# Kernel tuning notes

Measured on AMD Instinct MI355X. Metric: run time of the kernel, lower is better.

The kernel has to match this reference:

```python
import jax, jax.numpy as jnp
import numpy as np

N = 50000       # nodes
E = 800000      # edges (avg degree 16)
DIN = 128
DOUT = 128
ALPHA = 0.2     # leaky relu negative slope


def setup_inputs() -> dict:
    key = jax.random.key(0)
    k1, k2, k3, k4, k5 = jax.random.split(key, 5)
    h = jax.random.normal(k1, (N, DIN), dtype=jnp.float32)
    # xavier-normal-ish scaling for params
    W = jax.random.normal(k2, (DIN, DOUT), dtype=jnp.float32) * np.float32(np.sqrt(2.0 / (DIN + DOUT)))
    a = jax.random.normal(k3, (2 * DOUT,), dtype=jnp.float32) * np.float32(np.sqrt(2.0 / (2 * DOUT + 1)))
    src = jax.random.randint(k4, (E,), 0, N, dtype=jnp.int32)
    dst = jax.random.randint(k5, (E,), 0, N, dtype=jnp.int32)
    return {"h": h, "W": W, "a": a, "src": src, "dst": dst}


def reference(h, W, a, src, dst):
    # eval mode: dropout is a no-op (training=False)
    Wh = h @ W                                  # [N, DOUT]
    a_src, a_dst = a[:DOUT], a[DOUT:]
    s = Wh @ a_src                              # [N] per-node src score
    d = Wh @ a_dst                              # [N] per-node dst score
    e = jax.nn.leaky_relu(s[src] + d[dst], negative_slope=ALPHA)  # [E]
    # segment softmax over incoming edges of each dst node
    emax = jax.ops.segment_max(e, dst, num_segments=N)            # [N]
    emax = jnp.where(jnp.isfinite(emax), emax, jnp.float32(0.0))  # isolated nodes
    ex = jnp.exp(e - emax[dst])                                   # [E]
    denom = jax.ops.segment_sum(ex, dst, num_segments=N)          # [N]
    alpha = ex / denom[dst]                                       # [E]
    # weighted scatter-sum of src features into dst nodes
    h_out = jax.ops.segment_sum(alpha[:, None] * Wh[src], dst, num_segments=N)  # [N, DOUT]
    # residual: in_feats == out_feats -> Identity
    return h_out + h
```

## Files before the change

### kernel.cpp

```cpp
#include <hip/hip_runtime.h>
#include <math.h>

#define NN 50000
#define NE 800000
#define DD 128
#define LRELU 0.2f
#define CAP 64
#define SLICE 6256

typedef unsigned int uint;

__device__ __forceinline__ uint pack_bf2(float x, float y) {
  uint a = __float_as_uint(x), b = __float_as_uint(y);
  a = (a + 0x7fffu + ((a >> 16) & 1u)) >> 16;
  b = (b + 0x7fffu + ((b >> 16) & 1u)) >> 16;
  return a | (b << 16);
}

__global__ __launch_bounds__(256) void k_gemm(const float* __restrict__ h,
                                              const float* __restrict__ W,
                                              const float* __restrict__ a,
                                              uint* __restrict__ Whb,
                                              float* __restrict__ sv,
                                              float* __restrict__ dv,
                                              int* __restrict__ cnt) {
  __shared__ float hs[32][64];
  __shared__ float Ws[32][128];
  const int tid = threadIdx.x;
  const int brow = blockIdx.x * 64;

  if (tid < 64) {
    int idx = blockIdx.x * 64 + tid;
    if (idx < NN) cnt[idx] = 0;
  }

  const int tx = tid & 15, ty = tid >> 4;
  const int c0 = tx * 4, c1 = 64 + tx * 4;
  float acc[4][8];
#pragma unroll
  for (int r = 0; r < 4; ++r)
#pragma unroll
    for (int j = 0; j < 8; ++j) acc[r][j] = 0.f;

  const int lr = tid >> 2;
  const int lc = (tid & 3) * 8;
  int grow = brow + lr; if (grow >= NN) grow = 0;

  for (int k0 = 0; k0 < DD; k0 += 32) {
    {
      const float4* hp = reinterpret_cast<const float4*>(h + (size_t)grow * DD + k0 + lc);
      float4 v0 = hp[0], v1 = hp[1];
      hs[lc + 0][lr] = v0.x; hs[lc + 1][lr] = v0.y;
      hs[lc + 2][lr] = v0.z; hs[lc + 3][lr] = v0.w;
      hs[lc + 4][lr] = v1.x; hs[lc + 5][lr] = v1.y;
      hs[lc + 6][lr] = v1.z; hs[lc + 7][lr] = v1.w;
    }
#pragma unroll
    for (int i = 0; i < 4; ++i) {
      int f = i * 256 + tid;
      int kk = f >> 5, cc = (f & 31) * 4;
      *reinterpret_cast<float4*>(&Ws[kk][cc]) =
          *reinterpret_cast<const float4*>(W + (size_t)(k0 + kk) * DD + cc);
    }
    __syncthreads();
#pragma unroll
    for (int k = 0; k < 32; ++k) {
      float4 av = *reinterpret_cast<const float4*>(&hs[k][ty * 4]);
      float4 b0 = *reinterpret_cast<const float4*>(&Ws[k][c0]);
      float4 b1 = *reinterpret_cast<const float4*>(&Ws[k][c1]);
      acc[0][0] = fmaf(av.x, b0.x, acc[0][0]); acc[0][1] = fmaf(av.x, b0.y, acc[0][1]);
      acc[0][2] = fmaf(av.x, b0.z, acc[0][2]); acc[0][3] = fmaf(av.x, b0.w, acc[0][3]);
      acc[0][4] = fmaf(av.x, b1.x, acc[0][4]); acc[0][5] = fmaf(av.x, b1.y, acc[0][5]);
      acc[0][6] = fmaf(av.x, b1.z, acc[0][6]); acc[0][7] = fmaf(av.x, b1.w, acc[0][7]);
      acc[1][0] = fmaf(av.y, b0.x, acc[1][0]); acc[1][1] = fmaf(av.y, b0.y, acc[1][1]);
      acc[1][2] = fmaf(av.y, b0.z, acc[1][2]); acc[1][3] = fmaf(av.y, b0.w, acc[1][3]);
      acc[1][4] = fmaf(av.y, b1.x, acc[1][4]); acc[1][5] = fmaf(av.y, b1.y, acc[1][5]);
      acc[1][6] = fmaf(av.y, b1.z, acc[1][6]); acc[1][7] = fmaf(av.y, b1.w, acc[1][7]);
      acc[2][0] = fmaf(av.z, b0.x, acc[2][0]); acc[2][1] = fmaf(av.z, b0.y, acc[2][1]);
      acc[2][2] = fmaf(av.z, b0.z, acc[2][2]); acc[2][3] = fmaf(av.z, b0.w, acc[2][3]);
      acc[2][4] = fmaf(av.z, b1.x, acc[2][4]); acc[2][5] = fmaf(av.z, b1.y, acc[2][5]);
      acc[2][6] = fmaf(av.z, b1.z, acc[2][6]); acc[2][7] = fmaf(av.z, b1.w, acc[2][7]);
      acc[3][0] = fmaf(av.w, b0.x, acc[3][0]); acc[3][1] = fmaf(av.w, b0.y, acc[3][1]);
      acc[3][2] = fmaf(av.w, b0.z, acc[3][2]); acc[3][3] = fmaf(av.w, b0.w, acc[3][3]);
      acc[3][4] = fmaf(av.w, b1.x, acc[3][4]); acc[3][5] = fmaf(av.w, b1.y, acc[3][5]);
      acc[3][6] = fmaf(av.w, b1.z, acc[3][6]); acc[3][7] = fmaf(av.w, b1.w, acc[3][7]);
    }
    __syncthreads();
  }

  float4 as0 = *reinterpret_cast<const float4*>(a + c0);
  float4 as1 = *reinterpret_cast<const float4*>(a + c1);
  float4 ad0 = *reinterpret_cast<const float4*>(a + DD + c0);
  float4 ad1 = *reinterpret_cast<const float4*>(a + DD + c1);
#pragma unroll
  for (int r = 0; r < 4; ++r) {
    int row = brow + ty * 4 + r;
    bool ok = row < NN;
    if (ok) {
      uint2 p0 = make_uint2(pack_bf2(acc[r][0], acc[r][1]), pack_bf2(acc[r][2], acc[r][3]));
      uint2 p1 = make_uint2(pack_bf2(acc[r][4], acc[r][5]), pack_bf2(acc[r][6], acc[r][7]));
      *reinterpret_cast<uint2*>(Whb + (size_t)row * 64 + c0 / 2) = p0;
      *reinterpret_cast<uint2*>(Whb + (size_t)row * 64 + c1 / 2) = p1;
    }
    float ps = acc[r][0] * as0.x + acc[r][1] * as0.y + acc[r][2] * as0.z + acc[r][3] * as0.w
             + acc[r][4] * as1.x + acc[r][5] * as1.y + acc[r][6] * as1.z + acc[r][7] * as1.w;
    float pd = acc[r][0] * ad0.x + acc[r][1] * ad0.y + acc[r][2] * ad0.z + acc[r][3] * ad0.w
             + acc[r][4] * ad1.x + acc[r][5] * ad1.y + acc[r][6] * ad1.z + acc[r][7] * ad1.w;
#pragma unroll
    for (int off = 8; off > 0; off >>= 1) {
      ps += __shfl_xor(ps, off);
      pd += __shfl_xor(pd, off);
    }
    if (tx == 0 && ok) { sv[row] = ps; dv[row] = pd; }
  }
}

__global__ __launch_bounds__(256) void k_fill(const int* __restrict__ src,
                                              const int* __restrict__ dst,
                                              const float* __restrict__ sv,
                                              const float* __restrict__ dv,
                                              int* __restrict__ cnt,
                                              uint2* __restrict__ entries) {
  const int xcd = blockIdx.x & 7;
  const int e0 = (blockIdx.x >> 3) * 3125;
  const int e1 = e0 + 3125;
  for (int i = e0 + threadIdx.x; i < e1; i += 256) {
    int d = dst[i];
    if (d / SLICE != xcd) continue;
    int s = src[i];
    float ev = sv[s] + dv[d];
    ev = ev > 0.f ? ev : LRELU * ev;
    float x = __expf(ev);
    int p = atomicAdd(&cnt[d], 1);
    if (p < CAP) entries[(size_t)d * CAP + p] = make_uint2((uint)s, __float_as_uint(x));
  }
}

__global__ __launch_bounds__(256) void k_node(const float* __restrict__ h,
                                              const uint* __restrict__ Whb,
                                              const int* __restrict__ cnt,
                                              const uint2* __restrict__ entries,
                                              float* __restrict__ out) {
  const int sl = blockIdx.x & 7;
  int wid = sl * SLICE + (blockIdx.x >> 3) * 4 + (threadIdx.x >> 6);
  const int lim = min(NN, (sl + 1) * SLICE);
  if (wid >= lim) return;
  wid = __builtin_amdgcn_readfirstlane(wid);
  const int lane = threadIdx.x & 63;

  float2 hrow = reinterpret_cast<const float2*>(h + (size_t)wid * DD)[lane];
  int deg = cnt[wid];
  deg = deg < CAP ? deg : CAP;
  float2* o2 = reinterpret_cast<float2*>(out + (size_t)wid * DD);
  if (deg == 0) { o2[lane] = hrow; return; }

  const uint2* bucket = entries + (size_t)wid * CAP;
  float2 accA = make_float2(0.f, 0.f);
  float2 accB = make_float2(0.f, 0.f);
  float den = 0.f;
  int k = 0;
  for (; k + 2 <= deg; k += 2) {
    uint2 q0 = bucket[k], q1 = bucket[k + 1];
    float x0 = __uint_as_float(q0.y), x1 = __uint_as_float(q1.y);
    den += x0 + x1;
    uint u0 = Whb[(size_t)q0.x * 64 + lane];
    uint u1 = Whb[(size_t)q1.x * 64 + lane];
    accA.x = fmaf(x0, __uint_as_float(u0 << 16), accA.x);
    accA.y = fmaf(x0, __uint_as_float(u0 & 0xffff0000u), accA.y);
    accB.x = fmaf(x1, __uint_as_float(u1 << 16), accB.x);
    accB.y = fmaf(x1, __uint_as_float(u1 & 0xffff0000u), accB.y);
  }
  if (k < deg) {
    uint2 q0 = bucket[k];
    float x0 = __uint_as_float(q0.y);
    den += x0;
    uint u0 = Whb[(size_t)q0.x * 64 + lane];
    accA.x = fmaf(x0, __uint_as_float(u0 << 16), accA.x);
    accA.y = fmaf(x0, __uint_as_float(u0 & 0xffff0000u), accA.y);
  }
  float inv = 1.0f / den;
  o2[lane] = make_float2(hrow.x + (accA.x + accB.x) * inv,
                         hrow.y + (accA.y + accB.y) * inv);
}

extern "C" void kernel_launch(void* const* d_in, const int* in_sizes, int n_in,
                              void* d_out, int out_size, void* d_ws, size_t ws_size,
                              hipStream_t stream) {
  const float* h = (const float*)d_in[0];
  const float* W = (const float*)d_in[1];
  const float* a = (const float*)d_in[2];
  const int* src = (const int*)d_in[3];
  const int* dst = (const int*)d_in[4];
  float* out = (float*)d_out;

  char* ws = (char*)d_ws;
  uint*  Whb     = (uint*) (ws);
  float* sv      = (float*)(ws + 12800000);
  float* dv      = (float*)(ws + 13000000);
  int*   cnt     = (int*)  (ws + 13200000);
  uint2* entries = (uint2*)(ws + 13400000);

  hipLaunchKernelGGL(k_gemm, dim3((NN + 63) / 64), dim3(256), 0, stream,
                     h, W, a, Whb, sv, dv, cnt);
  hipLaunchKernelGGL(k_fill, dim3(2048), dim3(256), 0, stream,
                     src, dst, sv, dv, cnt, entries);
  hipLaunchKernelGGL(k_node, dim3(8 * ((SLICE + 3) / 4)), dim3(256), 0, stream,
                     h, Whb, cnt, entries, out);
}
```

Baseline: 185.5 us.

## Split GEMM into bf16 MFMA kernel, precompute W·a scores, compress edge entries

The FP32 shared-memory GEMM is replaced by several kernels. A single-block prep folds W·a into per-feature score vectors and writes a transposed bf16 copy of W. A light kernel computes the src/dst scores directly from h and casts h to bf16. A new kernel computes Wh with bf16 MFMA 16x16x32 instructions, reading W from swizzled LDS. Edge entries shrink to 4 bytes, holding a 16-bit source index and a bf16 exp weight, and k_fill and k_node are unrolled by 4 for more memory-level parallelism. This lowers GEMM and entry traffic at the cost of precision, an extra pass over h, and a serial single-block prep kernel. The 16-bit index relies on N being at most 65536.

```diff
diff --git a/kernel.cpp b/kernel.cpp
--- a/kernel.cpp
+++ b/kernel.cpp
@@ -9,6 +9,9 @@
 #define SLICE 6256
 
 typedef unsigned int uint;
+typedef unsigned short ushort;
+using short8 = __attribute__((ext_vector_type(8))) short;
+using f32x4  = __attribute__((ext_vector_type(4))) float;
 
 __device__ __forceinline__ uint pack_bf2(float x, float y) {
   uint a = __float_as_uint(x), b = __float_as_uint(y);
@@ -16,102 +19,123 @@
   b = (b + 0x7fffu + ((b >> 16) & 1u)) >> 16;
   return a | (b << 16);
 }
-
-__global__ __launch_bounds__(256) void k_gemm(const float* __restrict__ h,
-                                              const float* __restrict__ W,
+__device__ __forceinline__ ushort pack_bf1(float x) {
+  uint a = __float_as_uint(x);
+  return (ushort)((a + 0x7fffu + ((a >> 16) & 1u)) >> 16);
+}
+
+__global__ __launch_bounds__(256) void k_prep(const float* __restrict__ W,
                                               const float* __restrict__ a,
-                                              uint* __restrict__ Whb,
+                                              float* __restrict__ wsv,
+                                              float* __restrict__ wdv,
+                                              ushort* __restrict__ Wtg) {
+  const int tid = threadIdx.x;
+  if (tid < DD) {
+    float accs = 0.f, accd = 0.f;
+    for (int c = 0; c < DD; ++c) {
+      float w = W[tid * DD + c];
+      accs = fmaf(w, a[c], accs);
+      accd = fmaf(w, a[DD + c], accd);
+    }
+    wsv[tid] = accs;
+    wdv[tid] = accd;
+  }
+  for (int i = 0; i < 64; ++i) {
+    int idx = tid * 64 + i;
+    int c = idx >> 7, k = idx & 127;
+    Wtg[idx] = pack_bf1(W[k * DD + c]);
+  }
+}
+
+__global__ __launch_bounds__(256) void k_svdv(const float* __restrict__ h,
+                                              const float* __restrict__ wsv,
+                                              const float* __restrict__ wdv,
                                               float* __restrict__ sv,
                                               float* __restrict__ dv,
+                                              ushort* __restrict__ h_b,
                                               int* __restrict__ cnt) {
-  __shared__ float hs[32][64];
-  __shared__ float Ws[32][128];
   const int tid = threadIdx.x;
-  const int brow = blockIdx.x * 64;
-
-  if (tid < 64) {
-    int idx = blockIdx.x * 64 + tid;
-    if (idx < NN) cnt[idx] = 0;
-  }
-
-  const int tx = tid & 15, ty = tid >> 4;
-  const int c0 = tx * 4, c1 = 64 + tx * 4;
-  float acc[4][8];
-#pragma unroll
-  for (int r = 0; r < 4; ++r)
-#pragma unroll
-    for (int j = 0; j < 8; ++j) acc[r][j] = 0.f;
-
-  const int lr = tid >> 2;
-  const int lc = (tid & 3) * 8;
-  int grow = brow + lr; if (grow >= NN) grow = 0;
-
-  for (int k0 = 0; k0 < DD; k0 += 32) {
-    {
-      const float4* hp = reinterpret_cast<const float4*>(h + (size_t)grow * DD + k0 + lc);
-      float4 v0 = hp[0], v1 = hp[1];
-      hs[lc + 0][lr] = v0.x; hs[lc + 1][lr] = v0.y;
-      hs[lc + 2][lr] = v0.z; hs[lc + 3][lr] = v0.w;
-      hs[lc + 4][lr] = v1.x; hs[lc + 5][lr] = v1.y;
-      hs[lc + 6][lr] = v1.z; hs[lc + 7][lr] = v1.w;
-    }
-#pragma unroll
-    for (int i = 0; i < 4; ++i) {
-      int f = i * 256 + tid;
-      int kk = f >> 5, cc = (f & 31) * 4;
-      *reinterpret_cast<float4*>(&Ws[kk][cc]) =
-          *reinterpret_cast<const float4*>(W + (size_t)(k0 + kk) * DD + cc);
-    }
-    __syncthreads();
-#pragma unroll
-    for (int k = 0; k < 32; ++k) {
-      float4 av = *reinterpret_cast<const float4*>(&hs[k][ty * 4]);
-      float4 b0 = *reinterpret_cast<const float4*>(&Ws[k][c0]);
-      float4 b1 = *reinterpret_cast<const float4*>(&Ws[k][c1]);
-      acc[0][0] = fmaf(av.x, b0.x, acc[0][0]); acc[0][1] = fmaf(av.x, b0.y, acc[0][1]);
-      acc[0][2] = fmaf(av.x, b0.z, acc[0][2]); acc[0][3] = fmaf(av.x, b0.w, acc[0][3]);
-      acc[0][4] = fmaf(av.x, b1.x, acc[0][4]); acc[0][5] = fmaf(av.x, b1.y, acc[0][5]);
-      acc[0][6] = fmaf(av.x, b1.z, acc[0][6]); acc[0][7] = fmaf(av.x, b1.w, acc[0][7]);
-      acc[1][0] = fmaf(av.y, b0.x, acc[1][0]); acc[1][1] = fmaf(av.y, b0.y, acc[1][1]);
-      acc[1][2] = fmaf(av.y, b0.z, acc[1][2]); acc[1][3] = fmaf(av.y, b0.w, acc[1][3]);
-      acc[1][4] = fmaf(av.y, b1.x, acc[1][4]); acc[1][5] = fmaf(av.y, b1.y, acc[1][5]);
-      acc[1][6] = fmaf(av.y, b1.z, acc[1][6]); acc[1][7] = fmaf(av.y, b1.w, acc[1][7]);
-      acc[2][0] = fmaf(av.z, b0.x, acc[2][0]); acc[2][1] = fmaf(av.z, b0.y, acc[2][1]);
-      acc[2][2] = fmaf(av.z, b0.z, acc[2][2]); acc[2][3] = fmaf(av.z, b0.w, acc[2][3]);
-      acc[2][4] = fmaf(av.z, b1.x, acc[2][4]); acc[2][5] = fmaf(av.z, b1.y, acc[2][5]);
-      acc[2][6] = fmaf(av.z, b1.z, acc[2][6]); acc[2][7] = fmaf(av.z, b1.w, acc[2][7]);
-      acc[3][0] = fmaf(av.w, b0.x, acc[3][0]); acc[3][1] = fmaf(av.w, b0.y, acc[3][1]);
-      acc[3][2] = fmaf(av.w, b0.z, acc[3][2]); acc[3][3] = fmaf(av.w, b0.w, acc[3][3]);
-      acc[3][4] = fmaf(av.w, b1.x, acc[3][4]); acc[3][5] = fmaf(av.w, b1.y, acc[3][5]);
-      acc[3][6] = fmaf(av.w, b1.z, acc[3][6]); acc[3][7] = fmaf(av.w, b1.w, acc[3][7]);
-    }
-    __syncthreads();
-  }
-
-  float4 as0 = *reinterpret_cast<const float4*>(a + c0);
-  float4 as1 = *reinterpret_cast<const float4*>(a + c1);
-  float4 ad0 = *reinterpret_cast<const float4*>(a + DD + c0);
-  float4 ad1 = *reinterpret_cast<const float4*>(a + DD + c1);
-#pragma unroll
-  for (int r = 0; r < 4; ++r) {
-    int row = brow + ty * 4 + r;
-    bool ok = row < NN;
-    if (ok) {
-      uint2 p0 = make_uint2(pack_bf2(acc[r][0], acc[r][1]), pack_bf2(acc[r][2], acc[r][3]));
-      uint2 p1 = make_uint2(pack_bf2(acc[r][4], acc[r][5]), pack_bf2(acc[r][6], acc[r][7]));
-      *reinterpret_cast<uint2*>(Whb + (size_t)row * 64 + c0 / 2) = p0;
-      *reinterpret_cast<uint2*>(Whb + (size_t)row * 64 + c1 / 2) = p1;
-    }
-    float ps = acc[r][0] * as0.x + acc[r][1] * as0.y + acc[r][2] * as0.z + acc[r][3] * as0.w
-             + acc[r][4] * as1.x + acc[r][5] * as1.y + acc[r][6] * as1.z + acc[r][7] * as1.w;
-    float pd = acc[r][0] * ad0.x + acc[r][1] * ad0.y + acc[r][2] * ad0.z + acc[r][3] * ad0.w
-             + acc[r][4] * ad1.x + acc[r][5] * ad1.y + acc[r][6] * ad1.z + acc[r][7] * ad1.w;
-#pragma unroll
-    for (int off = 8; off > 0; off >>= 1) {
-      ps += __shfl_xor(ps, off);
-      pd += __shfl_xor(pd, off);
-    }
-    if (tx == 0 && ok) { sv[row] = ps; dv[row] = pd; }
+  if (tid < 16) cnt[blockIdx.x * 16 + tid] = 0;
+  const int wave = tid >> 6, l = tid & 63;
+  const int r = blockIdx.x * 16 + wave * 4 + (l >> 4);
+  const int c8 = (l & 15) * 8;
+  float4 h0 = *reinterpret_cast<const float4*>(h + (size_t)r * DD + c8);
+  float4 h1 = *reinterpret_cast<const float4*>(h + (size_t)r * DD + c8 + 4);
+  float4 w0 = *reinterpret_cast<const float4*>(wsv + c8);
+  float4 w1 = *reinterpret_cast<const float4*>(wsv + c8 + 4);
+  float4 d0 = *reinterpret_cast<const float4*>(wdv + c8);
+  float4 d1 = *reinterpret_cast<const float4*>(wdv + c8 + 4);
+  float ps = h0.x*w0.x + h0.y*w0.y + h0.z*w0.z + h0.w*w0.w
+           + h1.x*w1.x + h1.y*w1.y + h1.z*w1.z + h1.w*w1.w;
+  float pd = h0.x*d0.x + h0.y*d0.y + h0.z*d0.z + h0.w*d0.w
+           + h1.x*d1.x + h1.y*d1.y + h1.z*d1.z + h1.w*d1.w;
+#pragma unroll
+  for (int off = 1; off < 16; off <<= 1) {
+    ps += __shfl_xor(ps, off);
+    pd += __shfl_xor(pd, off);
+  }
+  if ((l & 15) == 0) { sv[r] = ps; dv[r] = pd; }
+  uint4 u;
+  u.x = pack_bf2(h0.x, h0.y); u.y = pack_bf2(h0.z, h0.w);
+  u.z = pack_bf2(h1.x, h1.y); u.w = pack_bf2(h1.z, h1.w);
+  *reinterpret_cast<uint4*>(h_b + (size_t)r * DD + c8) = u;
+}
+
+__global__ __launch_bounds__(256) void k_mfma(const ushort* __restrict__ h_b,
+                                              const ushort* __restrict__ Wtg,
+                                              uint* __restrict__ Whb) {
+  __shared__ ushort WtS[16384];
+  __shared__ float stage[4][16][18];
+  const int tid = threadIdx.x;
+
+#pragma unroll
+  for (int it = 0; it < 16; ++it) {
+    int chunk = it * 256 + tid;
+    int c = chunk >> 4, kc = chunk & 15;
+    short8 v = *reinterpret_cast<const short8*>(Wtg + chunk * 8);
+    *reinterpret_cast<short8*>(
+        reinterpret_cast<char*>(WtS) + c * 256 + ((kc ^ (c & 7)) << 4)) = v;
+  }
+  __syncthreads();
+
+  const int wave = tid >> 6, lane = tid & 63;
+  const int rbase = blockIdx.x * 64 + wave * 16;
+  const int arow = rbase + (lane & 15);
+  const int asrc = arow < NN ? arow : 0;
+  const bool rok = arow < NN;
+
+  short8 afr[4];
+#pragma unroll
+  for (int kg = 0; kg < 4; ++kg)
+    afr[kg] = *reinterpret_cast<const short8*>(
+        h_b + (size_t)asrc * DD + kg * 32 + (lane >> 4) * 8);
+
+  const int xb = lane & 7;
+  for (int cb = 0; cb < 8; ++cb) {
+    const int col = cb * 16 + (lane & 15);
+    f32x4 acc = {0.f, 0.f, 0.f, 0.f};
+#pragma unroll
+    for (int kg = 0; kg < 4; ++kg) {
+      int kchunk = kg * 4 + (lane >> 4);
+      short8 bfr = *reinterpret_cast<const short8*>(
+          reinterpret_cast<const char*>(WtS) + col * 256 + ((kchunk ^ xb) << 4));
+      acc = __builtin_amdgcn_mfma_f32_16x16x32_bf16(afr[kg], bfr, acc, 0, 0, 0);
+    }
+    float (*st)[18] = stage[wave];
+#pragma unroll
+    for (int j = 0; j < 4; ++j) st[(lane >> 4) * 4 + j][lane & 15] = acc[j];
+    __asm__ volatile("s_waitcnt lgkmcnt(0)" ::: "memory");
+    __builtin_amdgcn_sched_barrier(0);
+    if (rok) {
+#pragma unroll
+      for (int j2 = 0; j2 < 2; ++j2) {
+        int p = (lane >> 4) + 4 * j2;
+        float2 v = *reinterpret_cast<const float2*>(&st[lane & 15][2 * p]);
+        Whb[(size_t)arow * 64 + cb * 8 + p] = pack_bf2(v.x, v.y);
+      }
+    }
+    __asm__ volatile("s_waitcnt lgkmcnt(0)" ::: "memory");
+    __builtin_amdgcn_sched_barrier(0);
   }
 }
 
@@ -120,26 +144,52 @@
                                               const float* __restrict__ sv,
                                               const float* __restrict__ dv,
                                               int* __restrict__ cnt,
-                                              uint2* __restrict__ entries) {
+                                              uint* __restrict__ entries) {
   const int xcd = blockIdx.x & 7;
+  const int base = xcd * SLICE;
   const int e0 = (blockIdx.x >> 3) * 3125;
   const int e1 = e0 + 3125;
-  for (int i = e0 + threadIdx.x; i < e1; i += 256) {
-    int d = dst[i];
-    if (d / SLICE != xcd) continue;
-    int s = src[i];
-    float ev = sv[s] + dv[d];
-    ev = ev > 0.f ? ev : LRELU * ev;
-    float x = __expf(ev);
-    int p = atomicAdd(&cnt[d], 1);
-    if (p < CAP) entries[(size_t)d * CAP + p] = make_uint2((uint)s, __float_as_uint(x));
+  const int t = threadIdx.x;
+
+  for (int j0 = 0; j0 < 13; j0 += 4) {
+    int idx[4], d[4];
+    bool keep[4];
+#pragma unroll
+    for (int jj = 0; jj < 4; ++jj) {
+      idx[jj] = e0 + (j0 + jj) * 256 + t;
+      bool valid = idx[jj] < e1;
+      d[jj] = valid ? dst[idx[jj]] : -1;
+      keep[jj] = valid && ((uint)(d[jj] - base) < (uint)SLICE);
+    }
+    int s[4];
+    float x[4];
+#pragma unroll
+    for (int jj = 0; jj < 4; ++jj)
+      s[jj] = keep[jj] ? src[idx[jj]] : 0;
+#pragma unroll
+    for (int jj = 0; jj < 4; ++jj) {
+      if (keep[jj]) {
+        float ev = sv[s[jj]] + dv[d[jj]];
+        ev = ev > 0.f ? ev : LRELU * ev;
+        x[jj] = __expf(ev);
+      }
+    }
+    int p[4];
+#pragma unroll
+    for (int jj = 0; jj < 4; ++jj)
+      if (keep[jj]) p[jj] = atomicAdd(&cnt[d[jj]], 1);
+#pragma unroll
+    for (int jj = 0; jj < 4; ++jj)
+      if (keep[jj] && p[jj] < CAP)
+        entries[(size_t)d[jj] * CAP + p[jj]] =
+            ((uint)pack_bf1(x[jj]) << 16) | (uint)s[jj];
   }
 }
 
 __global__ __launch_bounds__(256) void k_node(const float* __restrict__ h,
                                               const uint* __restrict__ Whb,
                                               const int* __restrict__ cnt,
-                                              const uint2* __restrict__ entries,
+                                              const uint* __restrict__ entries,
                                               float* __restrict__ out) {
   const int sl = blockIdx.x & 7;
   int wid = sl * SLICE + (blockIdx.x >> 3) * 4 + (threadIdx.x >> 6);
@@ -154,33 +204,43 @@
   float2* o2 = reinterpret_cast<float2*>(out + (size_t)wid * DD);
   if (deg == 0) { o2[lane] = hrow; return; }
 
-  const uint2* bucket = entries + (size_t)wid * CAP;
-  float2 accA = make_float2(0.f, 0.f);
-  float2 accB = make_float2(0.f, 0.f);
+  const uint* bucket = entries + (size_t)wid * CAP;
+  const uint4* b4 = reinterpret_cast<const uint4*>(bucket);
+  float2 ac0 = {0.f,0.f}, ac1 = {0.f,0.f}, ac2 = {0.f,0.f}, ac3 = {0.f,0.f};
   float den = 0.f;
-  int k = 0;
-  for (; k + 2 <= deg; k += 2) {
-    uint2 q0 = bucket[k], q1 = bucket[k + 1];
-    float x0 = __uint_as_float(q0.y), x1 = __uint_as_float(q1.y);
-    den += x0 + x1;
-    uint u0 = Whb[(size_t)q0.x * 64 + lane];
-    uint u1 = Whb[(size_t)q1.x * 64 + lane];
-    accA.x = fmaf(x0, __uint_as_float(u0 << 16), accA.x);
-    accA.y = fmaf(x0, __uint_as_float(u0 & 0xffff0000u), accA.y);
-    accB.x = fmaf(x1, __uint_as_float(u1 << 16), accB.x);
-    accB.y = fmaf(x1, __uint_as_float(u1 & 0xffff0000u), accB.y);
-  }
-  if (k < deg) {
-    uint2 q0 = bucket[k];
-    float x0 = __uint_as_float(q0.y);
+  const int nq = deg >> 2;
+  for (int q = 0; q < nq; ++q) {
+    uint4 e4 = b4[q];
+    float x0 = __uint_as_float(e4.x & 0xffff0000u);
+    float x1 = __uint_as_float(e4.y & 0xffff0000u);
+    float x2 = __uint_as_float(e4.z & 0xffff0000u);
+    float x3 = __uint_as_float(e4.w & 0xffff0000u);
+    uint u0 = Whb[(size_t)(e4.x & 0xffffu) * 64 + lane];
+    uint u1 = Whb[(size_t)(e4.y & 0xffffu) * 64 + lane];
+    uint u2 = Whb[(size_t)(e4.z & 0xffffu) * 64 + lane];
+    uint u3 = Whb[(size_t)(e4.w & 0xffffu) * 64 + lane];
+    den += (x0 + x1) + (x2 + x3);
+    ac0.x = fmaf(x0, __uint_as_float(u0 << 16), ac0.x);
+    ac0.y = fmaf(x0, __uint_as_float(u0 & 0xffff0000u), ac0.y);
+    ac1.x = fmaf(x1, __uint_as_float(u1 << 16), ac1.x);
+    ac1.y = fmaf(x1, __uint_as_float(u1 & 0xffff0000u), ac1.y);
+    ac2.x = fmaf(x2, __uint_as_float(u2 << 16), ac2.x);
+    ac2.y = fmaf(x2, __uint_as_float(u2 & 0xffff0000u), ac2.y);
+    ac3.x = fmaf(x3, __uint_as_float(u3 << 16), ac3.x);
+    ac3.y = fmaf(x3, __uint_as_float(u3 & 0xffff0000u), ac3.y);
+  }
+  for (int k = nq * 4; k < deg; ++k) {
+    uint e = bucket[k];
+    float x0 = __uint_as_float(e & 0xffff0000u);
+    uint u0 = Whb[(size_t)(e & 0xffffu) * 64 + lane];
     den += x0;
-    uint u0 = Whb[(size_t)q0.x * 64 + lane];
-    accA.x = fmaf(x0, __uint_as_float(u0 << 16), accA.x);
-    accA.y = fmaf(x0, __uint_as_float(u0 & 0xffff0000u), accA.y);
+    ac0.x = fmaf(x0, __uint_as_float(u0 << 16), ac0.x);
+    ac0.y = fmaf(x0, __uint_as_float(u0 & 0xffff0000u), ac0.y);
   }
   float inv = 1.0f / den;
-  o2[lane] = make_float2(hrow.x + (accA.x + accB.x) * inv,
-                         hrow.y + (accA.y + accB.y) * inv);
+  float ax = (ac0.x + ac1.x) + (ac2.x + ac3.x);
+  float ay = (ac0.y + ac1.y) + (ac2.y + ac3.y);
+  o2[lane] = make_float2(hrow.x + ax * inv, hrow.y + ay * inv);
 }
 
 extern "C" void kernel_launch(void* const* d_in, const int* in_sizes, int n_in,
@@ -194,16 +254,22 @@
   float* out = (float*)d_out;
 
   char* ws = (char*)d_ws;
-  uint*  Whb     = (uint*) (ws);
-  float* sv      = (float*)(ws + 12800000);
-  float* dv      = (float*)(ws + 13000000);
-  int*   cnt     = (int*)  (ws + 13200000);
-  uint2* entries = (uint2*)(ws + 13400000);
-
-  hipLaunchKernelGGL(k_gemm, dim3((NN + 63) / 64), dim3(256), 0, stream,
-                     h, W, a, Whb, sv, dv, cnt);
+  uint*   Whb     = (uint*)  (ws);
+  ushort* h_b     = (ushort*)(ws + 12800000);
+  uint*   entries = (uint*)  (ws + 25600000);
+  ushort* Wtg     = (ushort*)(ws + 38400000);
+  float*  sv      = (float*) (ws + 38432768);
+  float*  dv      = (float*) (ws + 38632768);
+  float*  wsv     = (float*) (ws + 38832768);
+  float*  wdv     = (float*) (ws + 38833280);
+  int*    cnt     = (int*)   (ws + 38833792);
+
+  hipLaunchKernelGGL(k_prep, dim3(1), dim3(256), 0, stream, W, a, wsv, wdv, Wtg);
+  hipLaunchKernelGGL(k_svdv, dim3(3125), dim3(256), 0, stream,
+                     h, wsv, wdv, sv, dv, h_b, cnt);
   hipLaunchKernelGGL(k_fill, dim3(2048), dim3(256), 0, stream,
                      src, dst, sv, dv, cnt, entries);
-  hipLaunchKernelGGL(k_node, dim3(8 * ((SLICE + 3) / 4)), dim3(256), 0, stream,
+  hipLaunchKernelGGL(k_mfma, dim3(782), dim3(256), 0, stream, h_b, Wtg, Whb);
+  hipLaunchKernelGGL(k_node, dim3(8 * (SLICE / 4)), dim3(256), 0, stream,
                      h, Whb, cnt, entries, out);
 }
```

Result: no change. 185.8 us (+0.1%).
